# Performance work log

Measured on AMD Instinct MI355X. Metric: run time of the kernel, lower is better.

## Reference

```python
import jax, jax.numpy as jnp
import numpy as np

NUM_GROUPS = 32
EPS = 1e-5


def setup_inputs() -> dict:
    key = jax.random.key(0)
    ks = jax.random.split(key, 3)
    B, C, H, W = 4, 128, 64, 64
    x = jax.random.normal(ks[0], (B, C, H, W), dtype=jnp.float32)
    norm_w = jnp.ones((C,), jnp.float32)
    norm_b = jnp.zeros((C,), jnp.float32)
    qkv_w = jax.random.normal(ks[1], (3 * C, C), dtype=jnp.float32) * (C ** -0.5)
    qkv_b = jnp.zeros((3 * C,), jnp.float32)
    proj_w = jax.random.normal(ks[2], (C, C), dtype=jnp.float32) * (C ** -0.5)
    proj_b = jnp.zeros((C,), jnp.float32)
    return {"x": x, "norm_w": norm_w, "norm_b": norm_b,
            "qkv_w": qkv_w, "qkv_b": qkv_b,
            "proj_w": proj_w, "proj_b": proj_b}


def group_norm(x, w, b):
    B, C, H, W = x.shape
    xg = x.reshape(B, NUM_GROUPS, -1)  # [B, G, (C/G)*H*W]
    mean = jnp.mean(xg, axis=-1, keepdims=True)
    var = jnp.var(xg, axis=-1, keepdims=True)
    h = ((xg - mean) * jax.lax.rsqrt(var + EPS)).reshape(B, C, H, W)
    return h * w[None, :, None, None] + b[None, :, None, None]


def reference(x, norm_w, norm_b, qkv_w, qkv_b, proj_w, proj_b):
    B, C, H, W = x.shape
    N = H * W
    scale = C ** -0.5
    h = group_norm(x, norm_w, norm_b)
    # 1x1 conv == per-pixel matmul over channels
    qkv = jnp.einsum('bchw,dc->bdhw', h, qkv_w) + qkv_b[None, :, None, None]
    q, k, v = jnp.split(qkv.reshape(B, 3 * C, N), 3, axis=1)  # each [B, C, N]
    attn = jax.nn.softmax(jnp.einsum('bcn,bcm->bnm', q, k) * scale, axis=-1)  # [B,N,N]
    out = jnp.einsum('bnm,bcm->bcn', attn, v).reshape(B, C, H, W)
    out = jnp.einsum('bchw,dc->bdhw', out, proj_w) + proj_b[None, :, None, None]
    return x + out
```

## Files before the change

kernel.cpp:

```cpp
#include <hip/hip_runtime.h>
#include <hip/hip_bf16.h>

typedef __attribute__((ext_vector_type(8))) short short8_t;
typedef __attribute__((ext_vector_type(4))) float f32x4_t;
typedef __attribute__((ext_vector_type(16))) float f32x16_t;
typedef __attribute__((ext_vector_type(2))) unsigned int uint2v_t;
typedef __attribute__((ext_vector_type(4))) unsigned int uint4v_t;

#define MFMA16(a, b, c) __builtin_amdgcn_mfma_f32_16x16x32_bf16((a), (b), (c), 0, 0, 0)
#define MFMA32(a, b, c) __builtin_amdgcn_mfma_f32_32x32x16_bf16((a), (b), (c), 0, 0, 0)

__device__ __forceinline__ unsigned short f2bf(float f) {
  unsigned int u = __float_as_uint(f);
  unsigned int r = (u + 0x7fffu + ((u >> 16) & 1u)) >> 16;
  return (unsigned short)r;
}
__device__ __forceinline__ float bf2f(unsigned short u) {
  return __uint_as_float(((unsigned int)u) << 16);
}

__device__ __forceinline__ unsigned int cvt_pk_bf16(float lo, float hi) {
  unsigned int r;
  asm("v_cvt_pk_bf16_f32 %0, %1, %2" : "=v"(r) : "v"(lo), "v"(hi));
  return r;
}

__device__ __forceinline__ float ex2(float x) {
  float r;
  asm("v_exp_f32 %0, %1" : "=v"(r) : "v"(x));
  return r;
}

__device__ __forceinline__ void gload_lds16(const void* g, void* l) {
  __builtin_amdgcn_global_load_lds(
      (const __attribute__((address_space(1))) unsigned int*)g,
      (__attribute__((address_space(3))) unsigned int*)l, 16, 0, 0);
}

template <int ROWBYTES>
__device__ __forceinline__ void stage_swz(const char* __restrict__ g, int gstride,
                                          char* lds, int nrows, int tid, int nthr) {
  constexpr int CPR = ROWBYTES / 16;
  int chunks = nrows * CPR;
  for (int i = tid; i < chunks; i += nthr) {
    int row = i / CPR;
    int bc = (i - row * CPR) << 4;
    uint4 val = *(const uint4*)(g + (size_t)row * gstride + bc);
    *(uint4*)(lds + row * ROWBYTES + (bc ^ ((row & 7) << 4))) = val;
  }
}

#define NB 4
#define NC 128
#define NN 4096
#define NG 32
#define NS 6
#define ATT_SCALE 0.08838834764831843f
#define QSCALE (0.08838834764831843f * 1.4426950408889634f)
#define FIXED_MAX2 14.426950408889634f

__global__ __launch_bounds__(256) void gn_stats(const float* __restrict__ x,
                                                float* __restrict__ mean,
                                                float* __restrict__ rstd) {
  int bg = blockIdx.x;
  const float4* p = (const float4*)(x + (size_t)bg * 16384);
  float s = 0.f, ss = 0.f;
  for (int i = threadIdx.x; i < 4096; i += 256) {
    float4 v = p[i];
    s += v.x + v.y + v.z + v.w;
    ss += v.x * v.x + v.y * v.y + v.z * v.z + v.w * v.w;
  }
#pragma unroll
  for (int off = 32; off >= 1; off >>= 1) {
    s += __shfl_down(s, off);
    ss += __shfl_down(ss, off);
  }
  __shared__ float sb[4], ssb[4];
  int w = threadIdx.x >> 6;
  if ((threadIdx.x & 63) == 0) { sb[w] = s; ssb[w] = ss; }
  __syncthreads();
  if (threadIdx.x == 0) {
    float ts = sb[0] + sb[1] + sb[2] + sb[3];
    float tss = ssb[0] + ssb[1] + ssb[2] + ssb[3];
    float m = ts * (1.f / 16384.f);
    float var = tss * (1.f / 16384.f) - m * m;
    mean[bg] = m;
    rstd[bg] = rsqrtf(var + 1e-5f);
  }
}

__global__ __launch_bounds__(256) void gn_apply_t(const float* __restrict__ x,
                                                  const float* __restrict__ mean,
                                                  const float* __restrict__ rstd,
                                                  const float* __restrict__ gw,
                                                  const float* __restrict__ gb,
                                                  unsigned short* __restrict__ h_t) {
  int b = blockIdx.y;
  int n0 = blockIdx.x * 32;
  __shared__ float tile[128][33];
  const float* xb = x + (size_t)b * NC * NN;
  for (int i = threadIdx.x; i < 4096; i += 256) {
    int c = i >> 5, n = i & 31;
    int g = c >> 2;
    float v = xb[(size_t)c * NN + n0 + n];
    v = (v - mean[b * NG + g]) * rstd[b * NG + g];
    tile[c][n] = v * gw[c] + gb[c];
  }
  __syncthreads();
  unsigned short* out = h_t + ((size_t)b * NN + n0) * NC;
  for (int i = threadIdx.x; i < 4096; i += 256) {
    int n = i >> 7, c = i & 127;
    out[n * NC + c] = f2bf(tile[c][n]);
  }
}

__global__ __launch_bounds__(256) void conv_w(const float* __restrict__ qkv_w,
                                              const float* __restrict__ proj_w,
                                              unsigned short* __restrict__ wq,
                                              unsigned short* __restrict__ wp) {
  int i = blockIdx.x * 256 + threadIdx.x;
  if (i < 384 * 128) wq[i] = f2bf(qkv_w[i]);
  if (i < 128 * 128) wp[i] = f2bf(proj_w[i]);
}

template <int MODE>
__global__ __launch_bounds__(256) void bt_gemm(const unsigned short* __restrict__ Abf,
                                               const unsigned short* __restrict__ Bbf,
                                               const float* __restrict__ lp,
                                               const float* __restrict__ bias,
                                               const float* __restrict__ xres,
                                               unsigned short* __restrict__ q_t,
                                               unsigned short* __restrict__ k_t,
                                               unsigned short* __restrict__ v,
                                               float* __restrict__ out) {
  __shared__ __align__(16) char As[128 * 256];
  __shared__ __align__(16) char Bs[64 * 256];
  __shared__ float invl[64];
  int nt = blockIdx.x, dt = blockIdx.y, b = blockIdx.z;
  int tid = threadIdx.x;
  stage_swz<256>((const char*)(Abf + (size_t)dt * 128 * NC), 256, As, 128, tid, 256);
  if (MODE == 0) {
    stage_swz<256>((const char*)(Bbf + ((size_t)b * NN + nt * 64) * NC), 256, Bs, 64, tid, 256);
  } else {
    if (tid < 64) {
      float ls = 0.f;
#pragma unroll
      for (int s2 = 0; s2 < NS; ++s2)
        ls += lp[(size_t)(b * NS + s2) * NN + nt * 64 + tid];
      invl[tid] = 1.f / ls;
    }
    for (int i = tid; i < 64 * 16; i += 256) {
      int row = i >> 4, sl = i & 15;
      float f[8] = {};
#pragma unroll
      for (int s2 = 0; s2 < NS; ++s2) {
        const unsigned short* p =
            Bbf + ((size_t)(b * NS + s2) * NN + nt * 64 + row) * 128 + sl * 8;
        ushort4 u0 = *(const ushort4*)p;
        ushort4 u1 = *(const ushort4*)(p + 4);
        f[0] += bf2f(u0.x); f[1] += bf2f(u0.y); f[2] += bf2f(u0.z); f[3] += bf2f(u0.w);
        f[4] += bf2f(u1.x); f[5] += bf2f(u1.y); f[6] += bf2f(u1.z); f[7] += bf2f(u1.w);
      }
      uint4 packed;
      packed.x = (unsigned int)f2bf(f[0]) | ((unsigned int)f2bf(f[1]) << 16);
      packed.y = (unsigned int)f2bf(f[2]) | ((unsigned int)f2bf(f[3]) << 16);
      packed.z = (unsigned int)f2bf(f[4]) | ((unsigned int)f2bf(f[5]) << 16);
      packed.w = (unsigned int)f2bf(f[6]) | ((unsigned int)f2bf(f[7]) << 16);
      *(uint4*)(Bs + row * 256 + ((sl << 4) ^ ((row & 7) << 4))) = packed;
    }
  }
  __syncthreads();

  int l = tid & 63, w = tid >> 6;
  f32x4_t acc[2][4] = {};
  int arow0 = w * 32 + (l & 15);
  int brow0 = (l & 15);
  int kbyte0 = (l >> 4) * 16;
#pragma unroll
  for (int kk = 0; kk < 4; ++kk) {
    int kb = kk * 64 + kbyte0;
    short8_t aF[2], bF[4];
#pragma unroll
    for (int mi = 0; mi < 2; ++mi) {
      int r = arow0 + mi * 16;
      aF[mi] = *(const short8_t*)(As + r * 256 + (kb ^ ((r & 7) << 4)));
    }
#pragma unroll
    for (int ni = 0; ni < 4; ++ni) {
      int r = brow0 + ni * 16;
      bF[ni] = *(const short8_t*)(Bs + r * 256 + (kb ^ ((r & 7) << 4)));
    }
#pragma unroll
    for (int mi = 0; mi < 2; ++mi)
#pragma unroll
      for (int ni = 0; ni < 4; ++ni)
        acc[mi][ni] = MFMA16(aF[mi], bF[ni], acc[mi][ni]);
  }

  int rbase = (l >> 4) * 4;
  int cl = l & 15;
  float invl4[4];
  if (MODE == 1) {
#pragma unroll
    for (int ni = 0; ni < 4; ++ni) invl4[ni] = invl[ni * 16 + cl];
  }
#pragma unroll
  for (int mi = 0; mi < 2; ++mi) {
#pragma unroll
    for (int ni = 0; ni < 4; ++ni) {
      int n = nt * 64 + ni * 16 + cl;
#pragma unroll
      for (int r = 0; r < 4; ++r) {
        int d = dt * 128 + w * 32 + mi * 16 + rbase + r;
        if (MODE == 0) {
          float val = acc[mi][ni][r] + bias[d];
          if (dt == 0)
            q_t[((size_t)b * NN + n) * NC + d] = f2bf(val * QSCALE);
          else if (dt == 1)
            k_t[((size_t)b * NN + n) * NC + (d - 128)] = f2bf(val);
          else
            v[((size_t)b * NC + (d - 256)) * NN + n] = f2bf(val);
        } else {
          float val = acc[mi][ni][r] * invl4[ni] + bias[d];
          size_t idx = ((size_t)b * NC + d) * NN + n;
          out[idx] = xres[idx] + val;
        }
      }
    }
  }
}


__device__ __forceinline__ void issue_kv32(const char* __restrict__ gKt,
                                           const char* __restrict__ gVt,
                                           char* Kbuf, char* Vbuf, int wg, int lane) {
#pragma unroll
  for (int i = 0; i < 2; ++i) {
    int ci = wg * 2 + i;
    int row = ci * 4 + (lane >> 4);
    int col = (lane & 15) << 4;
    gload_lds16(gKt + row * 256 + (col ^ ((row & 7) << 4)), Kbuf + ci * 1024);
  }
#pragma unroll
  for (int i = 0; i < 2; ++i) {
    int ci = wg * 2 + i;
    int rowl = lane >> 3;
    int sl = (lane & 7) ^ rowl;
    int c = (ci * 8 + rowl) * 2 + (sl >> 2);
    int k16 = sl & 3;
    gload_lds16(gVt + (size_t)c * (NN * 2) + k16 * 16, Vbuf + ci * 1024);
  }
}

__global__ __launch_bounds__(256, 3) void attn(const unsigned short* __restrict__ q_t,
                                               const unsigned short* __restrict__ k_t,
                                               const unsigned short* __restrict__ v,
                                               unsigned short* __restrict__ O_p,
                                               float* __restrict__ l_p) {
  __shared__ __align__(16) char lds[32768];
  int qt = blockIdx.x, s = blockIdx.y, b = blockIdx.z;
  int tid = threadIdx.x, l = tid & 63, wg = tid >> 6;
  int ql = l & 31, qh = l >> 5;

  int t0 = 21 * s + min(s, 2);
  int cnt = 21 + (s < 2 ? 1 : 0);

  const char* gK = (const char*)(k_t + (size_t)b * NN * NC);
  const char* gV = (const char*)(v + (size_t)b * NC * NN);

  const unsigned short* gQ = q_t + ((size_t)b * NN + qt * 128 + wg * 32) * NC;
  short8_t bQ[8];
#pragma unroll
  for (int kk = 0; kk < 8; ++kk)
    bQ[kk] = *(const short8_t*)(gQ + (size_t)ql * NC + kk * 16 + qh * 8);

  issue_kv32(gK + (size_t)t0 * 8192, gV + (size_t)t0 * 64, lds, lds + 16384, wg, l);
  __syncthreads();

  f32x16_t oacc[4] = {};
  float lsum0 = 0.f, lsum1 = 0.f;

  for (int ti = 0; ti < cnt; ++ti) {
    int co = (ti & 1) << 13;
    int no = co ^ 8192;
    if (ti + 1 < cnt)
      issue_kv32(gK + (size_t)(t0 + ti + 1) * 8192, gV + (size_t)(t0 + ti + 1) * 64,
                 lds + no, lds + 16384 + no, wg, l);
    const char* Ks = lds + co;
    const char* Vs = lds + 16384 + co;

    f32x16_t sacc = {};
    __builtin_amdgcn_s_setprio(1);
#pragma unroll
    for (int kk = 0; kk < 8; ++kk) {
      short8_t aK = *(const short8_t*)(Ks + ql * 256 + ((kk * 32 + qh * 16) ^ ((ql & 7) << 4)));
      sacc = MFMA32(aK, bQ[kk], sacc);
    }
    __builtin_amdgcn_s_setprio(0);

    float p[16];
#pragma unroll
    for (int r = 0; r < 16; ++r) {
      p[r] = ex2(sacc[r] - FIXED_MAX2);
      if (r & 8) lsum1 += p[r]; else lsum0 += p[r];
    }

    unsigned int A0 = cvt_pk_bf16(p[0], p[1]), A1 = cvt_pk_bf16(p[2], p[3]);
    unsigned int B0 = cvt_pk_bf16(p[4], p[5]), B1 = cvt_pk_bf16(p[6], p[7]);
    unsigned int C0 = cvt_pk_bf16(p[8], p[9]), C1 = cvt_pk_bf16(p[10], p[11]);
    unsigned int D0 = cvt_pk_bf16(p[12], p[13]), D1 = cvt_pk_bf16(p[14], p[15]);
    uint2v_t r0 = __builtin_amdgcn_permlane32_swap(A0, B0, false, false);
    uint2v_t r1 = __builtin_amdgcn_permlane32_swap(A1, B1, false, false);
    uint2v_t r2 = __builtin_amdgcn_permlane32_swap(C0, D0, false, false);
    uint2v_t r3 = __builtin_amdgcn_permlane32_swap(C1, D1, false, false);
    uint4v_t pa0 = {r0.x, r1.x, r0.y, r1.y};
    uint4v_t pa1 = {r2.x, r3.x, r2.y, r3.y};
    short8_t PA0 = __builtin_bit_cast(short8_t, pa0);
    short8_t PA1 = __builtin_bit_cast(short8_t, pa1);

    __builtin_amdgcn_s_setprio(1);
#pragma unroll
    for (int cb = 0; cb < 4; ++cb) {
#pragma unroll
      for (int ks = 0; ks < 2; ++ks) {
        int c = cb * 32 + ql;
        int row = c >> 1;
        int sl = ((c & 1) << 2) | (ks << 1) | qh;
        int pp = sl ^ (row & 7);
        short8_t aV = *(const short8_t*)(Vs + row * 128 + pp * 16);
        oacc[cb] = MFMA32(ks ? PA1 : PA0, aV, oacc[cb]);
      }
    }
    __builtin_amdgcn_s_setprio(0);

    __syncthreads();
  }

  float lanesum = lsum0 + lsum1;
  lanesum += __shfl_xor(lanesum, 32);

  unsigned short* Ob = O_p + ((size_t)(b * NS + s) * NN + qt * 128 + wg * 32) * 128;
#pragma unroll
  for (int r = 0; r < 16; ++r) {
    int q = (r & 3) + 8 * (r >> 2) + 4 * qh;
#pragma unroll
    for (int cb = 0; cb < 4; ++cb)
      Ob[(size_t)q * 128 + cb * 32 + ql] = f2bf(oacc[cb][r]);
  }
  if (l < 32)
    l_p[(size_t)(b * NS + s) * NN + qt * 128 + wg * 32 + ql] = lanesum;
}

extern "C" void kernel_launch(void* const* d_in, const int* in_sizes, int n_in,
                              void* d_out, int out_size, void* d_ws, size_t ws_size,
                              hipStream_t stream) {
  const float* x = (const float*)d_in[0];
  const float* norm_w = (const float*)d_in[1];
  const float* norm_b = (const float*)d_in[2];
  const float* qkv_w = (const float*)d_in[3];
  const float* qkv_b = (const float*)d_in[4];
  const float* proj_w = (const float*)d_in[5];
  const float* proj_b = (const float*)d_in[6];
  float* out = (float*)d_out;

  char* ws = (char*)d_ws;
  float* mean = (float*)ws;
  float* rstd = (float*)(ws + 512);
  unsigned short* wq = (unsigned short*)(ws + 4096);
  unsigned short* wp = (unsigned short*)(ws + 4096 + 98304);
  const size_t TEN = (size_t)NB * NN * NC;
  unsigned short* h_t = (unsigned short*)(ws + (1 << 18));
  unsigned short* q_t = h_t + TEN;
  unsigned short* k_t = q_t + TEN;
  unsigned short* v = k_t + TEN;
  unsigned short* O_p = (unsigned short*)(ws + (1 << 18) + 4 * TEN * 2);
  float* l_p = (float*)((char*)O_p + (size_t)NS * NB * NN * NC * 2);

  gn_stats<<<NB * NG, 256, 0, stream>>>(x, mean, rstd);
  gn_apply_t<<<dim3(NN / 32, NB), 256, 0, stream>>>(x, mean, rstd, norm_w, norm_b, h_t);
  conv_w<<<192, 256, 0, stream>>>(qkv_w, proj_w, wq, wp);
  bt_gemm<0><<<dim3(NN / 64, 3, NB), 256, 0, stream>>>(wq, h_t, nullptr, qkv_b, nullptr,
                                                       q_t, k_t, v, nullptr);
  attn<<<dim3(NN / 128, NS, NB), 256, 0, stream>>>(q_t, k_t, v, O_p, l_p);
  bt_gemm<1><<<dim3(NN / 64, 1, NB), 256, 0, stream>>>(wp, O_p, l_p, proj_b, x,
                                                       nullptr, nullptr, nullptr, out);
}
```

Before: 82.04 us.

## Fuse group-norm apply into QKV GEMM and merge weight conversion with stats

```diff
diff --git a/kernel.cpp b/kernel.cpp
--- a/kernel.cpp
+++ b/kernel.cpp
@@ -37,16 +37,13 @@
       (__attribute__((address_space(3))) unsigned int*)l, 16, 0, 0);
 }
 
-template <int ROWBYTES>
-__device__ __forceinline__ void stage_swz(const char* __restrict__ g, int gstride,
-                                          char* lds, int nrows, int tid, int nthr) {
-  constexpr int CPR = ROWBYTES / 16;
-  int chunks = nrows * CPR;
-  for (int i = tid; i < chunks; i += nthr) {
-    int row = i / CPR;
-    int bc = (i - row * CPR) << 4;
-    uint4 val = *(const uint4*)(g + (size_t)row * gstride + bc);
-    *(uint4*)(lds + row * ROWBYTES + (bc ^ ((row & 7) << 4))) = val;
+__device__ __forceinline__ void stage_gload_256(const char* __restrict__ g,
+                                                char* lds, int nchunks,
+                                                int wg, int nw, int lane) {
+  for (int c = wg; c < nchunks; c += nw) {
+    int row = c * 4 + (lane >> 4);
+    int srco = row * 256 + ((((lane & 15) << 4)) ^ ((row & 7) << 4));
+    gload_lds16(g + srco, lds + c * 1024);
   }
 }
 
@@ -59,9 +56,19 @@
 #define QSCALE (0.08838834764831843f * 1.4426950408889634f)
 #define FIXED_MAX2 14.426950408889634f
 
-__global__ __launch_bounds__(256) void gn_stats(const float* __restrict__ x,
-                                                float* __restrict__ mean,
-                                                float* __restrict__ rstd) {
+__global__ __launch_bounds__(256) void gn_stats_convw(const float* __restrict__ x,
+                                                      const float* __restrict__ qkv_w,
+                                                      const float* __restrict__ proj_w,
+                                                      float* __restrict__ mean,
+                                                      float* __restrict__ rstd,
+                                                      unsigned short* __restrict__ wq,
+                                                      unsigned short* __restrict__ wp) {
+  if (blockIdx.x >= 128) {
+    int i = (blockIdx.x - 128) * 256 + threadIdx.x;
+    if (i < 384 * 128) wq[i] = f2bf(qkv_w[i]);
+    if (i < 128 * 128) wp[i] = f2bf(proj_w[i]);
+    return;
+  }
   int bg = blockIdx.x;
   const float4* p = (const float4*)(x + (size_t)bg * 16384);
   float s = 0.f, ss = 0.f;
@@ -89,89 +96,59 @@
   }
 }
 
-__global__ __launch_bounds__(256) void gn_apply_t(const float* __restrict__ x,
-                                                  const float* __restrict__ mean,
-                                                  const float* __restrict__ rstd,
-                                                  const float* __restrict__ gw,
-                                                  const float* __restrict__ gb,
-                                                  unsigned short* __restrict__ h_t) {
-  int b = blockIdx.y;
-  int n0 = blockIdx.x * 32;
-  __shared__ float tile[128][33];
-  const float* xb = x + (size_t)b * NC * NN;
-  for (int i = threadIdx.x; i < 4096; i += 256) {
-    int c = i >> 5, n = i & 31;
-    int g = c >> 2;
-    float v = xb[(size_t)c * NN + n0 + n];
-    v = (v - mean[b * NG + g]) * rstd[b * NG + g];
-    tile[c][n] = v * gw[c] + gb[c];
-  }
-  __syncthreads();
-  unsigned short* out = h_t + ((size_t)b * NN + n0) * NC;
-  for (int i = threadIdx.x; i < 4096; i += 256) {
-    int n = i >> 7, c = i & 127;
-    out[n * NC + c] = f2bf(tile[c][n]);
-  }
-}
-
-__global__ __launch_bounds__(256) void conv_w(const float* __restrict__ qkv_w,
-                                              const float* __restrict__ proj_w,
-                                              unsigned short* __restrict__ wq,
-                                              unsigned short* __restrict__ wp) {
-  int i = blockIdx.x * 256 + threadIdx.x;
-  if (i < 384 * 128) wq[i] = f2bf(qkv_w[i]);
-  if (i < 128 * 128) wp[i] = f2bf(proj_w[i]);
-}
-
-template <int MODE>
-__global__ __launch_bounds__(256) void bt_gemm(const unsigned short* __restrict__ Abf,
-                                               const unsigned short* __restrict__ Bbf,
-                                               const float* __restrict__ lp,
-                                               const float* __restrict__ bias,
-                                               const float* __restrict__ xres,
-                                               unsigned short* __restrict__ q_t,
-                                               unsigned short* __restrict__ k_t,
-                                               unsigned short* __restrict__ v,
-                                               float* __restrict__ out) {
+__global__ __launch_bounds__(256) void qkv_gemm(const float* __restrict__ x,
+                                                const float* __restrict__ mean,
+                                                const float* __restrict__ rstd,
+                                                const float* __restrict__ gw,
+                                                const float* __restrict__ gb,
+                                                const unsigned short* __restrict__ wq,
+                                                const float* __restrict__ bias,
+                                                unsigned short* __restrict__ q_t,
+                                                unsigned short* __restrict__ k_t,
+                                                unsigned short* __restrict__ v) {
   __shared__ __align__(16) char As[128 * 256];
   __shared__ __align__(16) char Bs[64 * 256];
-  __shared__ float invl[64];
+  __shared__ __align__(16) unsigned short T[128 * 72];
   int nt = blockIdx.x, dt = blockIdx.y, b = blockIdx.z;
-  int tid = threadIdx.x;
-  stage_swz<256>((const char*)(Abf + (size_t)dt * 128 * NC), 256, As, 128, tid, 256);
-  if (MODE == 0) {
-    stage_swz<256>((const char*)(Bbf + ((size_t)b * NN + nt * 64) * NC), 256, Bs, 64, tid, 256);
-  } else {
-    if (tid < 64) {
-      float ls = 0.f;
-#pragma unroll
-      for (int s2 = 0; s2 < NS; ++s2)
-        ls += lp[(size_t)(b * NS + s2) * NN + nt * 64 + tid];
-      invl[tid] = 1.f / ls;
-    }
-    for (int i = tid; i < 64 * 16; i += 256) {
-      int row = i >> 4, sl = i & 15;
-      float f[8] = {};
-#pragma unroll
-      for (int s2 = 0; s2 < NS; ++s2) {
-        const unsigned short* p =
-            Bbf + ((size_t)(b * NS + s2) * NN + nt * 64 + row) * 128 + sl * 8;
-        ushort4 u0 = *(const ushort4*)p;
-        ushort4 u1 = *(const ushort4*)(p + 4);
-        f[0] += bf2f(u0.x); f[1] += bf2f(u0.y); f[2] += bf2f(u0.z); f[3] += bf2f(u0.w);
-        f[4] += bf2f(u1.x); f[5] += bf2f(u1.y); f[6] += bf2f(u1.z); f[7] += bf2f(u1.w);
-      }
-      uint4 packed;
-      packed.x = (unsigned int)f2bf(f[0]) | ((unsigned int)f2bf(f[1]) << 16);
-      packed.y = (unsigned int)f2bf(f[2]) | ((unsigned int)f2bf(f[3]) << 16);
-      packed.z = (unsigned int)f2bf(f[4]) | ((unsigned int)f2bf(f[5]) << 16);
-      packed.w = (unsigned int)f2bf(f[6]) | ((unsigned int)f2bf(f[7]) << 16);
-      *(uint4*)(Bs + row * 256 + ((sl << 4) ^ ((row & 7) << 4))) = packed;
+  int tid = threadIdx.x, l = tid & 63, wgv = tid >> 6;
+  int n0 = nt * 64;
+
+  stage_gload_256((const char*)(wq + (size_t)dt * 128 * NC), As, 32, wgv, 4, l);
+
+  {
+    int c = tid >> 1, half = tid & 1;
+    int g = c >> 2;
+    float m = mean[b * NG + g], rs = rstd[b * NG + g];
+    float sc = gw[c] * rs, off = gb[c] - m * sc;
+    const float4* xr = (const float4*)(x + (size_t)b * NC * NN + (size_t)c * NN + n0 + half * 32);
+    unsigned short* tr = T + c * 72 + half * 32;
+#pragma unroll
+    for (int j = 0; j < 8; ++j) {
+      float4 vv = xr[j];
+      unsigned int p0 = (unsigned int)f2bf(vv.x * sc + off) |
+                        ((unsigned int)f2bf(vv.y * sc + off) << 16);
+      unsigned int p1 = (unsigned int)f2bf(vv.z * sc + off) |
+                        ((unsigned int)f2bf(vv.w * sc + off) << 16);
+      *(unsigned int*)(tr + j * 4) = p0;
+      *(unsigned int*)(tr + j * 4 + 2) = p1;
     }
   }
   __syncthreads();
 
-  int l = tid & 63, w = tid >> 6;
+  for (int u = tid; u < 1024; u += 256) {
+    int n = u >> 4, slot = u & 15;
+    int c0 = slot * 8;
+    uint4 packed;
+    unsigned int w0 = (unsigned int)T[(c0 + 0) * 72 + n] | ((unsigned int)T[(c0 + 1) * 72 + n] << 16);
+    unsigned int w1 = (unsigned int)T[(c0 + 2) * 72 + n] | ((unsigned int)T[(c0 + 3) * 72 + n] << 16);
+    unsigned int w2 = (unsigned int)T[(c0 + 4) * 72 + n] | ((unsigned int)T[(c0 + 5) * 72 + n] << 16);
+    unsigned int w3 = (unsigned int)T[(c0 + 6) * 72 + n] | ((unsigned int)T[(c0 + 7) * 72 + n] << 16);
+    packed.x = w0; packed.y = w1; packed.z = w2; packed.w = w3;
+    *(uint4*)(Bs + n * 256 + ((slot << 4) ^ ((n & 7) << 4))) = packed;
+  }
+  __syncthreads();
+
+  int w = tid >> 6;
   f32x4_t acc[2][4] = {};
   int arow0 = w * 32 + (l & 15);
   int brow0 = (l & 15);
@@ -199,11 +176,99 @@
 
   int rbase = (l >> 4) * 4;
   int cl = l & 15;
+#pragma unroll
+  for (int mi = 0; mi < 2; ++mi) {
+#pragma unroll
+    for (int ni = 0; ni < 4; ++ni) {
+      int n = n0 + ni * 16 + cl;
+#pragma unroll
+      for (int r = 0; r < 4; ++r) {
+        int d = dt * 128 + w * 32 + mi * 16 + rbase + r;
+        float val = acc[mi][ni][r] + bias[d];
+        if (dt == 0)
+          q_t[((size_t)b * NN + n) * NC + d] = f2bf(val * QSCALE);
+        else if (dt == 1)
+          k_t[((size_t)b * NN + n) * NC + (d - 128)] = f2bf(val);
+        else
+          v[((size_t)b * NC + (d - 256)) * NN + n] = f2bf(val);
+      }
+    }
+  }
+}
+
+__global__ __launch_bounds__(256) void proj_gemm(const unsigned short* __restrict__ wp,
+                                                 const unsigned short* __restrict__ O_p,
+                                                 const float* __restrict__ lp,
+                                                 const float* __restrict__ bias,
+                                                 const float* __restrict__ xres,
+                                                 float* __restrict__ out) {
+  __shared__ __align__(16) char As[128 * 256];
+  __shared__ __align__(16) char Bs[64 * 256];
+  __shared__ float invl[64];
+  int nt = blockIdx.x, b = blockIdx.z;
+  int tid = threadIdx.x, l = tid & 63, wgv = tid >> 6;
+
+  stage_gload_256((const char*)wp, As, 32, wgv, 4, l);
+
+  if (tid < 64) {
+    float ls = 0.f;
+#pragma unroll
+    for (int s2 = 0; s2 < NS; ++s2)
+      ls += lp[(size_t)(b * NS + s2) * NN + nt * 64 + tid];
+    invl[tid] = 1.f / ls;
+  }
+  for (int i = tid; i < 64 * 16; i += 256) {
+    int row = i >> 4, sl = i & 15;
+    float f[8] = {};
+#pragma unroll
+    for (int s2 = 0; s2 < NS; ++s2) {
+      const unsigned short* p =
+          O_p + ((size_t)(b * NS + s2) * NN + nt * 64 + row) * 128 + sl * 8;
+      ushort4 u0 = *(const ushort4*)p;
+      ushort4 u1 = *(const ushort4*)(p + 4);
+      f[0] += bf2f(u0.x); f[1] += bf2f(u0.y); f[2] += bf2f(u0.z); f[3] += bf2f(u0.w);
+      f[4] += bf2f(u1.x); f[5] += bf2f(u1.y); f[6] += bf2f(u1.z); f[7] += bf2f(u1.w);
+    }
+    uint4 packed;
+    packed.x = (unsigned int)f2bf(f[0]) | ((unsigned int)f2bf(f[1]) << 16);
+    packed.y = (unsigned int)f2bf(f[2]) | ((unsigned int)f2bf(f[3]) << 16);
+    packed.z = (unsigned int)f2bf(f[4]) | ((unsigned int)f2bf(f[5]) << 16);
+    packed.w = (unsigned int)f2bf(f[6]) | ((unsigned int)f2bf(f[7]) << 16);
+    *(uint4*)(Bs + row * 256 + ((sl << 4) ^ ((row & 7) << 4))) = packed;
+  }
+  __syncthreads();
+
+  int w = tid >> 6;
+  f32x4_t acc[2][4] = {};
+  int arow0 = w * 32 + (l & 15);
+  int brow0 = (l & 15);
+  int kbyte0 = (l >> 4) * 16;
+#pragma unroll
+  for (int kk = 0; kk < 4; ++kk) {
+    int kb = kk * 64 + kbyte0;
+    short8_t aF[2], bF[4];
+#pragma unroll
+    for (int mi = 0; mi < 2; ++mi) {
+      int r = arow0 + mi * 16;
+      aF[mi] = *(const short8_t*)(As + r * 256 + (kb ^ ((r & 7) << 4)));
+    }
+#pragma unroll
+    for (int ni = 0; ni < 4; ++ni) {
+      int r = brow0 + ni * 16;
+      bF[ni] = *(const short8_t*)(Bs + r * 256 + (kb ^ ((r & 7) << 4)));
+    }
+#pragma unroll
+    for (int mi = 0; mi < 2; ++mi)
+#pragma unroll
+      for (int ni = 0; ni < 4; ++ni)
+        acc[mi][ni] = MFMA16(aF[mi], bF[ni], acc[mi][ni]);
+  }
+
+  int rbase = (l >> 4) * 4;
+  int cl = l & 15;
   float invl4[4];
-  if (MODE == 1) {
-#pragma unroll
-    for (int ni = 0; ni < 4; ++ni) invl4[ni] = invl[ni * 16 + cl];
-  }
+#pragma unroll
+  for (int ni = 0; ni < 4; ++ni) invl4[ni] = invl[ni * 16 + cl];
 #pragma unroll
   for (int mi = 0; mi < 2; ++mi) {
 #pragma unroll
@@ -211,25 +276,14 @@
       int n = nt * 64 + ni * 16 + cl;
 #pragma unroll
       for (int r = 0; r < 4; ++r) {
-        int d = dt * 128 + w * 32 + mi * 16 + rbase + r;
-        if (MODE == 0) {
-          float val = acc[mi][ni][r] + bias[d];
-          if (dt == 0)
-            q_t[((size_t)b * NN + n) * NC + d] = f2bf(val * QSCALE);
-          else if (dt == 1)
-            k_t[((size_t)b * NN + n) * NC + (d - 128)] = f2bf(val);
-          else
-            v[((size_t)b * NC + (d - 256)) * NN + n] = f2bf(val);
-        } else {
-          float val = acc[mi][ni][r] * invl4[ni] + bias[d];
-          size_t idx = ((size_t)b * NC + d) * NN + n;
-          out[idx] = xres[idx] + val;
-        }
+        int d = w * 32 + mi * 16 + rbase + r;
+        float val = acc[mi][ni][r] * invl4[ni] + bias[d];
+        size_t idx = ((size_t)b * NC + d) * NN + n;
+        out[idx] = xres[idx] + val;
       }
     }
   }
 }
-
 
 __device__ __forceinline__ void issue_kv32(const char* __restrict__ gKt,
                                            const char* __restrict__ gVt,
@@ -369,19 +423,15 @@
   unsigned short* wq = (unsigned short*)(ws + 4096);
   unsigned short* wp = (unsigned short*)(ws + 4096 + 98304);
   const size_t TEN = (size_t)NB * NN * NC;
-  unsigned short* h_t = (unsigned short*)(ws + (1 << 18));
-  unsigned short* q_t = h_t + TEN;
+  unsigned short* q_t = (unsigned short*)(ws + (1 << 18));
   unsigned short* k_t = q_t + TEN;
   unsigned short* v = k_t + TEN;
-  unsigned short* O_p = (unsigned short*)(ws + (1 << 18) + 4 * TEN * 2);
+  unsigned short* O_p = (unsigned short*)(ws + (1 << 18) + 3 * TEN * 2);
   float* l_p = (float*)((char*)O_p + (size_t)NS * NB * NN * NC * 2);
 
-  gn_stats<<<NB * NG, 256, 0, stream>>>(x, mean, rstd);
-  gn_apply_t<<<dim3(NN / 32, NB), 256, 0, stream>>>(x, mean, rstd, norm_w, norm_b, h_t);
-  conv_w<<<192, 256, 0, stream>>>(qkv_w, proj_w, wq, wp);
-  bt_gemm<0><<<dim3(NN / 64, 3, NB), 256, 0, stream>>>(wq, h_t, nullptr, qkv_b, nullptr,
-                                                       q_t, k_t, v, nullptr);
+  gn_stats_convw<<<320, 256, 0, stream>>>(x, qkv_w, proj_w, mean, rstd, wq, wp);
+  qkv_gemm<<<dim3(NN / 64, 3, NB), 256, 0, stream>>>(x, mean, rstd, norm_w, norm_b,
+                                                     wq, qkv_b, q_t, k_t, v);
   attn<<<dim3(NN / 128, NS, NB), 256, 0, stream>>>(q_t, k_t, v, O_p, l_p);
-  bt_gemm<1><<<dim3(NN / 64, 1, NB), 256, 0, stream>>>(wp, O_p, l_p, proj_b, x,
-                                                       nullptr, nullptr, nullptr, out);
-}
+  proj_gemm<<<dim3(NN / 64, 1, NB), 256, 0, stream>>>(wp, O_p, l_p, proj_b, x, out);
+}
```

Measured after the change: 81.40 us. About the same (-0.8%).
